# Optimization experiments

Measured on AMD Instinct MI355X. Metric: run time of the kernel, lower is better.

## Reference

```python
import jax, jax.numpy as jnp
import numpy as np

N = 1024   # num nodes
D = 128    # feat_dim (input_dim)


def setup_inputs() -> dict:
    key = jax.random.key(0)
    k1, k2 = jax.random.split(key)
    x = jax.random.normal(k1, (N, D), dtype=jnp.float32)
    # nn.Linear(D, 1) -> weight vector [D], bias [1] (xavier init weight, zero bias)
    w_vec = jax.random.normal(k2, (D,), dtype=jnp.float32) * np.sqrt(2.0 / (D + 1))
    w_bias = jnp.zeros((1,), dtype=jnp.float32)
    return {"x": x, "w_vec": w_vec, "w_bias": w_bias}


def reference(x, w_vec, w_bias):
    # diff[i, j, d] = |x[i, d] - x[j, d]|  (repeat_interleave row-major -> x[i] minus broadcast x[j])
    diff = jnp.abs(x[:, None, :] - x[None, :, :])          # [N, N, D]
    scores = jnp.einsum('ijd,d->ij', diff, w_vec) + w_bias[0]  # Linear(D,1) -> [N, N]
    scores = jax.nn.relu(scores)
    return jax.nn.softmax(scores, axis=1)
```

## Files before the change

### kernel.cpp

```cpp
#include <hip/hip_runtime.h>

#define N 1024
#define D 128
#define PAD 132
#define MAGIC 0x3C96A5E1u

__global__ __launch_bounds__(256) void fused_kernel(
    const float* __restrict__ x, const float* __restrict__ w,
    const float* __restrict__ bias, float* __restrict__ S,
    unsigned int* __restrict__ ws) {
  __shared__ float sxi[64 * PAD];
  __shared__ float sxj[64 * PAD];

  unsigned int* flag    = ws;
  unsigned int* counter = ws + 32;
  float* rowsum = reinterpret_cast<float*>(ws) + 1024;

  const int t  = threadIdx.x;
  const int bi = blockIdx.y * 64;
  const int bj = blockIdx.x * 64;

  if (blockIdx.x == 0 && blockIdx.y == 0) {
    #pragma unroll
    for (int k = 0; k < 4; ++k)
      __hip_atomic_store(&rowsum[t * 4 + k], 0.0f, __ATOMIC_RELAXED,
                         __HIP_MEMORY_SCOPE_AGENT);
    if (t == 0)
      __hip_atomic_store(counter, 0u, __ATOMIC_RELAXED,
                         __HIP_MEMORY_SCOPE_AGENT);
    __syncthreads();
    __threadfence();
    if (t == 0)
      __hip_atomic_store(flag, MAGIC, __ATOMIC_RELEASE,
                         __HIP_MEMORY_SCOPE_AGENT);
  }

  {
    const int c  = t & 31;
    const int r0 = t >> 5;
    #pragma unroll
    for (int p = 0; p < 8; ++p) {
      const int r = r0 + p * 8;
      const float4 vi = reinterpret_cast<const float4*>(x)[(bi + r) * 32 + c];
      *reinterpret_cast<float4*>(&sxi[r * PAD + c * 4]) = vi;
      const float4 vj = reinterpret_cast<const float4*>(x)[(bj + r) * 32 + c];
      *reinterpret_cast<float4*>(&sxj[r * PAD + c * 4]) = vj;
    }
  }
  __syncthreads();

  const int tx = t & 15;
  const int ty = t >> 4;

  float acc[4][4];
  #pragma unroll
  for (int a = 0; a < 4; ++a)
    #pragma unroll
    for (int b = 0; b < 4; ++b) acc[a][b] = 0.f;

  #pragma unroll 2
  for (int d = 0; d < D; d += 4) {
    const float4 W = reinterpret_cast<const float4*>(w)[d >> 2];
    float4 A[4], B[4];
    #pragma unroll
    for (int a = 0; a < 4; ++a)
      A[a] = *reinterpret_cast<const float4*>(&sxi[(ty + 16 * a) * PAD + d]);
    #pragma unroll
    for (int b = 0; b < 4; ++b)
      B[b] = *reinterpret_cast<const float4*>(&sxj[(tx + 16 * b) * PAD + d]);

    #pragma unroll
    for (int a = 0; a < 4; ++a) {
      #pragma unroll
      for (int b = 0; b < 4; ++b) {
        float s = acc[a][b];
        s = fmaf(fabsf(A[a].x - B[b].x), W.x, s);
        s = fmaf(fabsf(A[a].y - B[b].y), W.y, s);
        s = fmaf(fabsf(A[a].z - B[b].z), W.z, s);
        s = fmaf(fabsf(A[a].w - B[b].w), W.w, s);
        acc[a][b] = s;
      }
    }
  }

  const float bv = bias[0];
  float e[4][4];
  float part[4];
  #pragma unroll
  for (int a = 0; a < 4; ++a) {
    float p = 0.f;
    #pragma unroll
    for (int b = 0; b < 4; ++b) {
      const float s  = fmaxf(acc[a][b] + bv, 0.f);
      const float ev = __expf(s);
      e[a][b] = ev;
      p += ev;
    }
    #pragma unroll
    for (int o = 1; o < 16; o <<= 1) p += __shfl_xor(p, o, 64);
    part[a] = p;
  }

  if (t == 0) {
    for (unsigned it = 0; it < (1u << 26); ++it) {
      if (__hip_atomic_load(flag, __ATOMIC_ACQUIRE,
                            __HIP_MEMORY_SCOPE_AGENT) == MAGIC) break;
      __builtin_amdgcn_s_sleep(2);
    }
  }
  __syncthreads();

  if (tx == 0) {
    #pragma unroll
    for (int a = 0; a < 4; ++a)
      atomicAdd(&rowsum[bi + ty + 16 * a], part[a]);
  }
  __syncthreads();

  if (t == 0) {
    __hip_atomic_fetch_add(counter, 1u, __ATOMIC_ACQ_REL,
                           __HIP_MEMORY_SCOPE_AGENT);
    for (unsigned it = 0; it < (1u << 26); ++it) {
      if (__hip_atomic_load(counter, __ATOMIC_ACQUIRE,
                            __HIP_MEMORY_SCOPE_AGENT) >= 256u) break;
      __builtin_amdgcn_s_sleep(2);
    }
  }
  __syncthreads();

  float rs[4];
  #pragma unroll
  for (int a = 0; a < 4; ++a)
    rs[a] = 1.0f / __hip_atomic_load(&rowsum[bi + ty + 16 * a],
                                     __ATOMIC_RELAXED, __HIP_MEMORY_SCOPE_AGENT);

  #pragma unroll
  for (int a = 0; a < 4; ++a) {
    const int row = bi + ty + 16 * a;
    #pragma unroll
    for (int b = 0; b < 4; ++b)
      S[row * N + bj + tx + 16 * b] = e[a][b] * rs[a];
  }
}

extern "C" void kernel_launch(void* const* d_in, const int* in_sizes, int n_in,
                              void* d_out, int out_size, void* d_ws, size_t ws_size,
                              hipStream_t stream) {
  const float* x = (const float*)d_in[0];
  const float* w = (const float*)d_in[1];
  const float* b = (const float*)d_in[2];
  float* out = (float*)d_out;
  unsigned int* ws = (unsigned int*)d_ws;

  dim3 grid(N / 64, N / 64);
  fused_kernel<<<grid, 256, 0, stream>>>(x, w, b, out, ws);
}
```

Measured before the change: 83.40 us.

## Halve column tile to 512 blocks and replace atomic rowsums with per-block partials

Shrinks the column tile from 64 to 32 so the grid grows from 256 to 512 blocks, spreading work over more CUs on the 256-CU device. Row-sum accumulation changes from float atomicAdd into a global rowsum to each block writing its partial into a dedicated slot, then reducing 32 partials per row after the grid barrier. This removes atomic contention and the rowsum zeroing, but each thread now does half the compute per shared load (a 4x2 register tile instead of 4x4). The barrier now depends on all 512 blocks being co-resident, and the spin limits are lowered.

```diff
diff --git a/kernel.cpp b/kernel.cpp
--- a/kernel.cpp
+++ b/kernel.cpp
@@ -4,35 +4,29 @@
 #define D 128
 #define PAD 132
 #define MAGIC 0x3C96A5E1u
+#define NBLK 512
 
 __global__ __launch_bounds__(256) void fused_kernel(
     const float* __restrict__ x, const float* __restrict__ w,
     const float* __restrict__ bias, float* __restrict__ S,
     unsigned int* __restrict__ ws) {
   __shared__ float sxi[64 * PAD];
-  __shared__ float sxj[64 * PAD];
+  __shared__ float sxj[32 * PAD];
+  __shared__ float srow[64];
 
   unsigned int* flag    = ws;
   unsigned int* counter = ws + 32;
-  float* rowsum = reinterpret_cast<float*>(ws) + 1024;
+  float* part = reinterpret_cast<float*>(ws) + 1024;
 
   const int t  = threadIdx.x;
   const int bi = blockIdx.y * 64;
-  const int bj = blockIdx.x * 64;
+  const int bj = blockIdx.x * 32;
+  const int cb = blockIdx.x;
 
-  if (blockIdx.x == 0 && blockIdx.y == 0) {
-    #pragma unroll
-    for (int k = 0; k < 4; ++k)
-      __hip_atomic_store(&rowsum[t * 4 + k], 0.0f, __ATOMIC_RELAXED,
-                         __HIP_MEMORY_SCOPE_AGENT);
-    if (t == 0)
-      __hip_atomic_store(counter, 0u, __ATOMIC_RELAXED,
-                         __HIP_MEMORY_SCOPE_AGENT);
-    __syncthreads();
+  if (blockIdx.x == 0 && blockIdx.y == 0 && t == 0) {
+    __hip_atomic_store(counter, 0u, __ATOMIC_RELAXED, __HIP_MEMORY_SCOPE_AGENT);
     __threadfence();
-    if (t == 0)
-      __hip_atomic_store(flag, MAGIC, __ATOMIC_RELEASE,
-                         __HIP_MEMORY_SCOPE_AGENT);
+    __hip_atomic_store(flag, MAGIC, __ATOMIC_RELEASE, __HIP_MEMORY_SCOPE_AGENT);
   }
 
   {
@@ -41,10 +35,14 @@
     #pragma unroll
     for (int p = 0; p < 8; ++p) {
       const int r = r0 + p * 8;
-      const float4 vi = reinterpret_cast<const float4*>(x)[(bi + r) * 32 + c];
-      *reinterpret_cast<float4*>(&sxi[r * PAD + c * 4]) = vi;
-      const float4 vj = reinterpret_cast<const float4*>(x)[(bj + r) * 32 + c];
-      *reinterpret_cast<float4*>(&sxj[r * PAD + c * 4]) = vj;
+      const float4 v = reinterpret_cast<const float4*>(x)[(bi + r) * 32 + c];
+      *reinterpret_cast<float4*>(&sxi[r * PAD + c * 4]) = v;
+    }
+    #pragma unroll
+    for (int p = 0; p < 4; ++p) {
+      const int r = r0 + p * 8;
+      const float4 v = reinterpret_cast<const float4*>(x)[(bj + r) * 32 + c];
+      *reinterpret_cast<float4*>(&sxj[r * PAD + c * 4]) = v;
     }
   }
   __syncthreads();
@@ -52,27 +50,27 @@
   const int tx = t & 15;
   const int ty = t >> 4;
 
-  float acc[4][4];
+  float acc[4][2];
   #pragma unroll
   for (int a = 0; a < 4; ++a)
     #pragma unroll
-    for (int b = 0; b < 4; ++b) acc[a][b] = 0.f;
+    for (int b = 0; b < 2; ++b) acc[a][b] = 0.f;
 
-  #pragma unroll 2
+  #pragma unroll 4
   for (int d = 0; d < D; d += 4) {
     const float4 W = reinterpret_cast<const float4*>(w)[d >> 2];
-    float4 A[4], B[4];
+    float4 A[4], B[2];
     #pragma unroll
     for (int a = 0; a < 4; ++a)
       A[a] = *reinterpret_cast<const float4*>(&sxi[(ty + 16 * a) * PAD + d]);
     #pragma unroll
-    for (int b = 0; b < 4; ++b)
+    for (int b = 0; b < 2; ++b)
       B[b] = *reinterpret_cast<const float4*>(&sxj[(tx + 16 * b) * PAD + d]);
 
     #pragma unroll
     for (int a = 0; a < 4; ++a) {
       #pragma unroll
-      for (int b = 0; b < 4; ++b) {
+      for (int b = 0; b < 2; ++b) {
         float s = acc[a][b];
         s = fmaf(fabsf(A[a].x - B[b].x), W.x, s);
         s = fmaf(fabsf(A[a].y - B[b].y), W.y, s);
@@ -84,13 +82,12 @@
   }
 
   const float bv = bias[0];
-  float e[4][4];
-  float part[4];
+  float e[4][2];
   #pragma unroll
   for (int a = 0; a < 4; ++a) {
     float p = 0.f;
     #pragma unroll
-    for (int b = 0; b < 4; ++b) {
+    for (int b = 0; b < 2; ++b) {
       const float s  = fmaxf(acc[a][b] + bv, 0.f);
       const float ev = __expf(s);
       e[a][b] = ev;
@@ -98,47 +95,52 @@
     }
     #pragma unroll
     for (int o = 1; o < 16; o <<= 1) p += __shfl_xor(p, o, 64);
-    part[a] = p;
+    if (tx == 0)
+      __hip_atomic_store(&part[(bi + ty + 16 * a) * 32 + cb], p,
+                         __ATOMIC_RELAXED, __HIP_MEMORY_SCOPE_AGENT);
   }
+  __syncthreads();
 
   if (t == 0) {
-    for (unsigned it = 0; it < (1u << 26); ++it) {
+    for (unsigned it = 0; it < (1u << 24); ++it) {
       if (__hip_atomic_load(flag, __ATOMIC_ACQUIRE,
                             __HIP_MEMORY_SCOPE_AGENT) == MAGIC) break;
+      __builtin_amdgcn_s_sleep(2);
+    }
+    __threadfence();
+    __hip_atomic_fetch_add(counter, 1u, __ATOMIC_ACQ_REL,
+                           __HIP_MEMORY_SCOPE_AGENT);
+    for (unsigned it = 0; it < (1u << 24); ++it) {
+      if (__hip_atomic_load(counter, __ATOMIC_ACQUIRE,
+                            __HIP_MEMORY_SCOPE_AGENT) >= NBLK) break;
       __builtin_amdgcn_s_sleep(2);
     }
   }
   __syncthreads();
 
-  if (tx == 0) {
+  {
+    const int r = t >> 2;
+    const int q = t & 3;
+    float s = 0.f;
     #pragma unroll
-    for (int a = 0; a < 4; ++a)
-      atomicAdd(&rowsum[bi + ty + 16 * a], part[a]);
-  }
-  __syncthreads();
-
-  if (t == 0) {
-    __hip_atomic_fetch_add(counter, 1u, __ATOMIC_ACQ_REL,
-                           __HIP_MEMORY_SCOPE_AGENT);
-    for (unsigned it = 0; it < (1u << 26); ++it) {
-      if (__hip_atomic_load(counter, __ATOMIC_ACQUIRE,
-                            __HIP_MEMORY_SCOPE_AGENT) >= 256u) break;
-      __builtin_amdgcn_s_sleep(2);
-    }
+    for (int k = 0; k < 8; ++k)
+      s += __hip_atomic_load(&part[(bi + r) * 32 + q * 8 + k],
+                             __ATOMIC_RELAXED, __HIP_MEMORY_SCOPE_AGENT);
+    s += __shfl_xor(s, 1, 64);
+    s += __shfl_xor(s, 2, 64);
+    if (q == 0) srow[r] = s;
   }
   __syncthreads();
 
   float rs[4];
   #pragma unroll
-  for (int a = 0; a < 4; ++a)
-    rs[a] = 1.0f / __hip_atomic_load(&rowsum[bi + ty + 16 * a],
-                                     __ATOMIC_RELAXED, __HIP_MEMORY_SCOPE_AGENT);
+  for (int a = 0; a < 4; ++a) rs[a] = 1.0f / srow[ty + 16 * a];
 
   #pragma unroll
   for (int a = 0; a < 4; ++a) {
     const int row = bi + ty + 16 * a;
     #pragma unroll
-    for (int b = 0; b < 4; ++b)
+    for (int b = 0; b < 2; ++b)
       S[row * N + bj + tx + 16 * b] = e[a][b] * rs[a];
   }
 }
@@ -152,6 +154,6 @@
   float* out = (float*)d_out;
   unsigned int* ws = (unsigned int*)d_ws;
 
-  dim3 grid(N / 64, N / 64);
+  dim3 grid(N / 32, N / 64);
   fused_kernel<<<grid, 256, 0, stream>>>(x, w, b, out, ws);
 }
```

New measurement: 104.0 us. 1.25x slower.

## Split D across four wave groups and replace grid-wide sync with a second kernel

Applied to the files above, without the earlier changes.

The fused kernel with spin-wait grid synchronisation becomes two kernels. The score kernel now uses 1024 threads per block, with four groups each reducing 32 of the 128 feature dims. Partial sums are combined through shared memory, and the kernel writes the unnormalized exponentials plus per-tile row partial sums. A separate scale kernel reduces the partials and normalizes each row. This removes the atomic flag and counter spin barrier and raises in-block parallelism, at the cost of an extra pass over the output and a second launch.

```diff
diff --git a/kernel.cpp b/kernel.cpp
--- a/kernel.cpp
+++ b/kernel.cpp
@@ -3,44 +3,25 @@
 #define N 1024
 #define D 128
 #define PAD 132
-#define MAGIC 0x3C96A5E1u
 
-__global__ __launch_bounds__(256) void fused_kernel(
+__global__ __launch_bounds__(1024, 4) void scores_kernel(
     const float* __restrict__ x, const float* __restrict__ w,
-    const float* __restrict__ bias, float* __restrict__ S,
-    unsigned int* __restrict__ ws) {
-  __shared__ float sxi[64 * PAD];
-  __shared__ float sxj[64 * PAD];
-
-  unsigned int* flag    = ws;
-  unsigned int* counter = ws + 32;
-  float* rowsum = reinterpret_cast<float*>(ws) + 1024;
+    const float* __restrict__ bias, float* __restrict__ E,
+    float* __restrict__ part) {
+  __shared__ float smem[2 * 64 * PAD];
+  float* sxi = smem;
+  float* sxj = smem + 64 * PAD;
 
   const int t  = threadIdx.x;
   const int bi = blockIdx.y * 64;
   const int bj = blockIdx.x * 64;
 
-  if (blockIdx.x == 0 && blockIdx.y == 0) {
-    #pragma unroll
-    for (int k = 0; k < 4; ++k)
-      __hip_atomic_store(&rowsum[t * 4 + k], 0.0f, __ATOMIC_RELAXED,
-                         __HIP_MEMORY_SCOPE_AGENT);
-    if (t == 0)
-      __hip_atomic_store(counter, 0u, __ATOMIC_RELAXED,
-                         __HIP_MEMORY_SCOPE_AGENT);
-    __syncthreads();
-    __threadfence();
-    if (t == 0)
-      __hip_atomic_store(flag, MAGIC, __ATOMIC_RELEASE,
-                         __HIP_MEMORY_SCOPE_AGENT);
-  }
-
   {
     const int c  = t & 31;
     const int r0 = t >> 5;
     #pragma unroll
-    for (int p = 0; p < 8; ++p) {
-      const int r = r0 + p * 8;
+    for (int p = 0; p < 2; ++p) {
+      const int r = r0 + p * 32;
       const float4 vi = reinterpret_cast<const float4*>(x)[(bi + r) * 32 + c];
       *reinterpret_cast<float4*>(&sxi[r * PAD + c * 4]) = vi;
       const float4 vj = reinterpret_cast<const float4*>(x)[(bj + r) * 32 + c];
@@ -49,8 +30,11 @@
   }
   __syncthreads();
 
-  const int tx = t & 15;
-  const int ty = t >> 4;
+  const int g  = __builtin_amdgcn_readfirstlane(t >> 8);
+  const int s  = t & 255;
+  const int tx = s & 15;
+  const int ty = s >> 4;
+  const int d0 = g * 32;
 
   float acc[4][4];
   #pragma unroll
@@ -59,8 +43,9 @@
     for (int b = 0; b < 4; ++b) acc[a][b] = 0.f;
 
   #pragma unroll 2
-  for (int d = 0; d < D; d += 4) {
-    const float4 W = reinterpret_cast<const float4*>(w)[d >> 2];
+  for (int dc = 0; dc < 8; ++dc) {
+    const float4 W = reinterpret_cast<const float4*>(w)[(d0 >> 2) + dc];
+    const int d = d0 + dc * 4;
     float4 A[4], B[4];
     #pragma unroll
     for (int a = 0; a < 4; ++a)
@@ -73,74 +58,72 @@
     for (int a = 0; a < 4; ++a) {
       #pragma unroll
       for (int b = 0; b < 4; ++b) {
-        float s = acc[a][b];
-        s = fmaf(fabsf(A[a].x - B[b].x), W.x, s);
-        s = fmaf(fabsf(A[a].y - B[b].y), W.y, s);
-        s = fmaf(fabsf(A[a].z - B[b].z), W.z, s);
-        s = fmaf(fabsf(A[a].w - B[b].w), W.w, s);
-        acc[a][b] = s;
+        float v = acc[a][b];
+        v = fmaf(fabsf(A[a].x - B[b].x), W.x, v);
+        v = fmaf(fabsf(A[a].y - B[b].y), W.y, v);
+        v = fmaf(fabsf(A[a].z - B[b].z), W.z, v);
+        v = fmaf(fabsf(A[a].w - B[b].w), W.w, v);
+        acc[a][b] = v;
       }
-    }
-  }
-
-  const float bv = bias[0];
-  float e[4][4];
-  float part[4];
-  #pragma unroll
-  for (int a = 0; a < 4; ++a) {
-    float p = 0.f;
-    #pragma unroll
-    for (int b = 0; b < 4; ++b) {
-      const float s  = fmaxf(acc[a][b] + bv, 0.f);
-      const float ev = __expf(s);
-      e[a][b] = ev;
-      p += ev;
-    }
-    #pragma unroll
-    for (int o = 1; o < 16; o <<= 1) p += __shfl_xor(p, o, 64);
-    part[a] = p;
-  }
-
-  if (t == 0) {
-    for (unsigned it = 0; it < (1u << 26); ++it) {
-      if (__hip_atomic_load(flag, __ATOMIC_ACQUIRE,
-                            __HIP_MEMORY_SCOPE_AGENT) == MAGIC) break;
-      __builtin_amdgcn_s_sleep(2);
     }
   }
   __syncthreads();
 
-  if (tx == 0) {
+  float* comb = smem;
+  if (g > 0) {
+    float* dst = comb + ((g - 1) * 256 + s) * 17;
     #pragma unroll
-    for (int a = 0; a < 4; ++a)
-      atomicAdd(&rowsum[bi + ty + 16 * a], part[a]);
+    for (int k = 0; k < 16; ++k) dst[k] = acc[k >> 2][k & 3];
   }
   __syncthreads();
 
-  if (t == 0) {
-    __hip_atomic_fetch_add(counter, 1u, __ATOMIC_ACQ_REL,
-                           __HIP_MEMORY_SCOPE_AGENT);
-    for (unsigned it = 0; it < (1u << 26); ++it) {
-      if (__hip_atomic_load(counter, __ATOMIC_ACQUIRE,
-                            __HIP_MEMORY_SCOPE_AGENT) >= 256u) break;
-      __builtin_amdgcn_s_sleep(2);
+  if (g == 0) {
+    #pragma unroll
+    for (int q = 0; q < 3; ++q) {
+      const float* src = comb + (q * 256 + s) * 17;
+      #pragma unroll
+      for (int k = 0; k < 16; ++k) acc[k >> 2][k & 3] += src[k];
+    }
+
+    const float bv = bias[0];
+    #pragma unroll
+    for (int a = 0; a < 4; ++a) {
+      float p = 0.f;
+      #pragma unroll
+      for (int b = 0; b < 4; ++b) {
+        const float ev = __expf(fmaxf(acc[a][b] + bv, 0.f));
+        acc[a][b] = ev;
+        p += ev;
+      }
+      #pragma unroll
+      for (int o = 1; o < 16; o <<= 1) p += __shfl_xor(p, o, 64);
+      if (tx == 0) part[(bi + ty + 16 * a) * 16 + blockIdx.x] = p;
+    }
+
+    #pragma unroll
+    for (int a = 0; a < 4; ++a) {
+      const int row = bi + ty + 16 * a;
+      #pragma unroll
+      for (int b = 0; b < 4; ++b)
+        E[row * N + bj + tx + 16 * b] = acc[a][b];
     }
   }
-  __syncthreads();
+}
 
-  float rs[4];
+__global__ __launch_bounds__(256) void scale_kernel(
+    float* __restrict__ S, const float* __restrict__ part) {
+  const int row = blockIdx.x;
+  const int t   = threadIdx.x;
+
+  float p = part[row * 16 + (t & 15)];
   #pragma unroll
-  for (int a = 0; a < 4; ++a)
-    rs[a] = 1.0f / __hip_atomic_load(&rowsum[bi + ty + 16 * a],
-                                     __ATOMIC_RELAXED, __HIP_MEMORY_SCOPE_AGENT);
+  for (int o = 1; o < 16; o <<= 1) p += __shfl_xor(p, o, 64);
+  const float r = 1.0f / p;
 
-  #pragma unroll
-  for (int a = 0; a < 4; ++a) {
-    const int row = bi + ty + 16 * a;
-    #pragma unroll
-    for (int b = 0; b < 4; ++b)
-      S[row * N + bj + tx + 16 * b] = e[a][b] * rs[a];
-  }
+  float4* rowp = reinterpret_cast<float4*>(S + row * N);
+  float4 v = rowp[t];
+  v.x *= r; v.y *= r; v.z *= r; v.w *= r;
+  rowp[t] = v;
 }
 
 extern "C" void kernel_launch(void* const* d_in, const int* in_sizes, int n_in,
@@ -149,9 +132,10 @@
   const float* x = (const float*)d_in[0];
   const float* w = (const float*)d_in[1];
   const float* b = (const float*)d_in[2];
-  float* out = (float*)d_out;
-  unsigned int* ws = (unsigned int*)d_ws;
+  float* out  = (float*)d_out;
+  float* part = (float*)d_ws;
 
   dim3 grid(N / 64, N / 64);
-  fused_kernel<<<grid, 256, 0, stream>>>(x, w, b, out, ws);
+  scores_kernel<<<grid, 1024, 0, stream>>>(x, w, b, out, part);
+  scale_kernel<<<N, 256, 0, stream>>>(out, part);
 }
```

New measurement: 75.26 us. 9.8% less time.
